# Performance work log

Hardware: AMD Instinct MI355X
Metric: run time of the kernel (lower is better)

Reference implementation:

```python
import jax, jax.numpy as jnp
import numpy as np

N = 100000          # nodes per type
D = 128             # embedding_dim
E_TREE = 100000     # intra-type tree edges
E_LINK = 1000000    # cross-type link edges
L = 2               # graph_num_layers
T = 4               # edge types: [dd, mm, dm, md]


def _sage(x_src, x_dst, ei, Wl, bl, Wr):
    """PyG SAGEConv(aggr='mean', normalize=False): lin_l(mean_j x_src_j) + lin_r(x_dst)."""
    n_dst = x_dst.shape[0]
    msg = x_src[ei[0]]                                                    # [E, D] gather
    ssum = jax.ops.segment_sum(msg, ei[1], num_segments=n_dst)            # [n_dst, D]
    cnt = jax.ops.segment_sum(jnp.ones((ei.shape[1],), x_src.dtype), ei[1], num_segments=n_dst)
    agg = ssum / jnp.maximum(cnt, 1.0)[:, None]                           # mean, safe for deg-0
    return agg @ Wl.T + bl + x_dst @ Wr.T


def _forward(x_d, x_m, e_dd, e_mm, e_dm, e_md, Wl, bl, Wr):
    num_layers = Wl.shape[0]
    for l in range(num_layers):
        # HeteroConv aggr='sum': sum conv outputs over edge types per dst node type
        nd = (_sage(x_d, x_d, e_dd, Wl[l, 0], bl[l, 0], Wr[l, 0])
              + _sage(x_m, x_d, e_md, Wl[l, 3], bl[l, 3], Wr[l, 3]))
        nm = (_sage(x_m, x_m, e_mm, Wl[l, 1], bl[l, 1], Wr[l, 1])
              + _sage(x_d, x_m, e_dm, Wl[l, 2], bl[l, 2], Wr[l, 2]))
        if l < num_layers - 1:
            nd, nm = jax.nn.relu(nd), jax.nn.relu(nm)
        x_d, x_m = nd, nm
    return jnp.stack([x_d, x_m])                                          # [2, N, D]


def setup_inputs() -> dict:
    key = jax.random.key(0)
    ks = jax.random.split(key, 9)
    scale = 1.0 / np.sqrt(D)
    return {
        "x_d": jax.random.normal(ks[0], (N, D), jnp.float32),
        "x_m": jax.random.normal(ks[1], (N, D), jnp.float32),
        "e_dd": jax.random.randint(ks[2], (2, E_TREE), 0, N, jnp.int64),
        "e_mm": jax.random.randint(ks[3], (2, E_TREE), 0, N, jnp.int64),
        "e_dm": jax.random.randint(ks[4], (2, E_LINK), 0, N, jnp.int64),
        "e_md": jax.random.randint(ks[5], (2, E_LINK), 0, N, jnp.int64),
        "Wl": jax.random.normal(ks[6], (L, T, D, D), jnp.float32) * scale,
        "bl": jax.random.normal(ks[7], (L, T, D), jnp.float32) * scale,
        "Wr": jax.random.normal(ks[8], (L, T, D, D), jnp.float32) * scale,
    }


def reference(x_d, x_m, e_dd, e_mm, e_dm, e_md, Wl, bl, Wr):
    return _forward(x_d, x_m, e_dd, e_mm, e_dm, e_md, Wl, bl, Wr)
```

## Files before the change

### kernel.cpp

```cpp
#include <hip/hip_runtime.h>

#define DD 128
#define KTOT 384
#define BM 64
#define BS_BITS 10
#define BS 1024
#define NBMAX 512
#define CHUNK 2048
#define CAP 12288

typedef __attribute__((ext_vector_type(8))) short short8;
typedef __attribute__((ext_vector_type(8))) unsigned short ushort8;
typedef __attribute__((ext_vector_type(4))) float floatx4;

__device__ __forceinline__ unsigned short f2b(float f) {
    union { float f; unsigned u; } v; v.f = f;
    return (unsigned short)((v.u + 0x7fffu + ((v.u >> 16) & 1u)) >> 16);
}
__device__ __forceinline__ float b2f(unsigned short u) {
    union { unsigned u; float f; } v; v.u = ((unsigned)u) << 16;
    return v.f;
}

__global__ __launch_bounds__(256) void detect_i32(const int* __restrict__ p, int nodd,
                                                  int* __restrict__ flag)
{
    int i = blockIdx.x * 256 + threadIdx.x;
    if (i < nodd && p[2 * i + 1] != 0) atomicOr(flag, 1);
}

__global__ __launch_bounds__(256) void cvt_bf16(const float* __restrict__ in,
                                                unsigned short* __restrict__ out, int n8)
{
    int i = blockIdx.x * 256 + threadIdx.x;
    if (i >= n8) return;
    float4 v0 = *(const float4*)(in + (size_t)i * 8);
    float4 v1 = *(const float4*)(in + (size_t)i * 8 + 4);
    ushort8 r;
    r[0]=f2b(v0.x); r[1]=f2b(v0.y); r[2]=f2b(v0.z); r[3]=f2b(v0.w);
    r[4]=f2b(v1.x); r[5]=f2b(v1.y); r[6]=f2b(v1.z); r[7]=f2b(v1.w);
    *(ushort8*)(out + (size_t)i * 8) = r;
}

__global__ __launch_bounds__(256) void build_wcomb(
    const float* __restrict__ Wl, const float* __restrict__ bl,
    const float* __restrict__ Wr, unsigned short* __restrict__ WTt, float* __restrict__ bc)
{
    int idx = blockIdx.x * 256 + threadIdx.x;
    if (idx < 2 * 2 * DD * KTOT) {
        int k  = idx % KTOT;
        int t1 = idx / KTOT;
        int i  = t1 & 127;
        int t2 = t1 >> 7;
        int dt = t2 & 1;
        int l  = t2 >> 1;
        int ta = dt ? 1 : 0;
        int tb = dt ? 2 : 3;
        float v;
        if (k < 128) {
            v = Wl[(((size_t)(l * 4 + ta) * 128 + i) << 7) + k];
        } else if (k < 256) {
            v = Wl[(((size_t)(l * 4 + tb) * 128 + i) << 7) + (k - 128)];
        } else {
            int kk = k - 256;
            v = Wr[(((size_t)(l * 4 + ta) * 128 + i) << 7) + kk]
              + Wr[(((size_t)(l * 4 + tb) * 128 + i) << 7) + kk];
        }
        int tidx = ((((i >> 4) * 12 + (k >> 5)) * 64) + (((k >> 3) & 3) * 16 + (i & 15))) * 8
                 + (k & 7);
        WTt[(size_t)t2 * (DD * KTOT) + tidx] = f2b(v);
    }
    if (idx < 512) {
        int i  = idx & 127;
        int t2 = idx >> 7;
        int dt = t2 & 1;
        int l  = t2 >> 1;
        int ta = dt ? 1 : 0;
        int tb = dt ? 2 : 3;
        bc[idx] = bl[(l * 4 + ta) * 128 + i] + bl[(l * 4 + tb) * 128 + i];
    }
}

__global__ __launch_bounds__(512) void bin_edges(
    const void* __restrict__ e0, const void* __restrict__ e1,
    const void* __restrict__ e2, const void* __restrict__ e3,
    int E0, int E1, int E2, int E3,
    const int* __restrict__ flag, int* __restrict__ bucket_fill,
    unsigned* __restrict__ stage,
    unsigned long long* __restrict__ ovf, int* __restrict__ ovf_cnt,
    int N, int nb)
{
    __shared__ unsigned sb_pack[CHUNK];
    __shared__ unsigned short sb_b[CHUNK];
    __shared__ int hist[NBMAX];
    __shared__ int offs[NBMAX];
    __shared__ int base[NBMAX];

    const int tid   = threadIdx.x;
    const int E_tot = E0 + E1 + E2 + E3;
    const int e_bas = blockIdx.x * CHUNK;
    const int e_end = min(e_bas + CHUNK, E_tot);
    const int cnt_e = e_end - e_bas;
    const int isI32 = *flag;

    for (int i = tid; i < nb; i += 512) hist[i] = 0;
    __syncthreads();

    unsigned my_pack[4];
    int my_b[4], my_r[4];
    #pragma unroll
    for (int u = 0; u < 4; ++u) {
        my_b[u] = -1;
        int e = e_bas + tid + u * 512;
        if (e < e_end) {
            const void* ep; int El, type, le = e;
            if (le < E0)              { ep = e0; El = E0; type = 0; }
            else if ((le -= E0) < E1) { ep = e1; El = E1; type = 1; }
            else if ((le -= E1) < E2) { ep = e2; El = E2; type = 2; }
            else                      { le -= E2; ep = e3; El = E3; type = 3; }
            int s, d;
            if (isI32) {
                s = ((const int*)ep)[le];
                d = ((const int*)ep)[(size_t)El + le];
            } else {
                s = (int)((const long long*)ep)[le];
                d = (int)((const long long*)ep)[(size_t)El + le];
            }
            int gnode = type * N + d;
            int b = gnode >> BS_BITS;
            my_b[u]    = b;
            my_pack[u] = ((unsigned)s << BS_BITS) | (unsigned)(gnode & (BS - 1));
            my_r[u]    = atomicAdd(&hist[b], 1);
        }
    }
    __syncthreads();

    offs[tid] = (tid < nb) ? hist[tid] : 0;
    __syncthreads();
    for (int d = 1; d < 512; d <<= 1) {
        int v = (tid >= d) ? offs[tid - d] : 0;
        __syncthreads();
        offs[tid] += v;
        __syncthreads();
    }
    if (tid < nb) {
        offs[tid] -= hist[tid];
        base[tid] = hist[tid] ? atomicAdd(&bucket_fill[tid], hist[tid]) : 0;
    }
    __syncthreads();

    #pragma unroll
    for (int u = 0; u < 4; ++u) {
        if (my_b[u] >= 0) {
            int pos = offs[my_b[u]] + my_r[u];
            sb_pack[pos] = my_pack[u];
            sb_b[pos]    = (unsigned short)my_b[u];
        }
    }
    __syncthreads();

    for (int pos = tid; pos < cnt_e; pos += 512) {
        int b = sb_b[pos];
        unsigned p = sb_pack[pos];
        int idx = base[b] + (pos - offs[b]);
        if (idx < CAP) {
            stage[(size_t)b * CAP + idx] = p;
        } else {
            int k = atomicAdd(ovf_cnt, 1);
            int gnode = (b << BS_BITS) | (int)(p & (BS - 1));
            ovf[k] = ((unsigned long long)(unsigned)gnode << 32) | (p >> BS_BITS);
        }
    }
}

__global__ __launch_bounds__(512) void scan_buckets(const int* __restrict__ fill, int nb,
                                                    int* __restrict__ base)
{
    __shared__ int s[512];
    const int tid = threadIdx.x;
    int v = (tid < nb) ? fill[tid] : 0;
    s[tid] = v;
    __syncthreads();
    for (int d = 1; d < 512; d <<= 1) {
        int u = (tid >= d) ? s[tid - d] : 0;
        __syncthreads();
        s[tid] += u;
        __syncthreads();
    }
    if (tid < nb) base[tid] = s[tid] - v;
}

__global__ __launch_bounds__(512) void fill_from_stage(
    const unsigned* __restrict__ stage, const int* __restrict__ bucket_fill,
    const int* __restrict__ bucket_base,
    const unsigned long long* __restrict__ ovf, const int* __restrict__ ovf_cnt,
    int* __restrict__ rp_all, float* __restrict__ inv_all, int* __restrict__ col, int n4)
{
    __shared__ int cl[BS];
    __shared__ int rl[BS];
    __shared__ int w[512];

    const int tid   = threadIdx.x;
    const int b     = blockIdx.x;
    const int node0 = b << BS_BITS;
    const int nn    = min(BS, n4 - node0);

    cl[tid] = 0; cl[tid + 512] = 0;
    __syncthreads();

    const int total  = bucket_fill[b];
    const int nstage = min(total, CAP);
    const unsigned* st = stage + (size_t)b * CAP;
    const int novf = *ovf_cnt;

    for (int j = tid; j < nstage; j += 512)
        atomicAdd(&cl[st[j] & (BS - 1)], 1);
    for (int k = tid; k < novf; k += 512) {
        int g = (int)(ovf[k] >> 32);
        if (g >= node0 && g < node0 + nn) atomicAdd(&cl[g - node0], 1);
    }
    __syncthreads();

    int a0 = cl[2 * tid], a1 = cl[2 * tid + 1];
    w[tid] = a0 + a1;
    __syncthreads();
    for (int d = 1; d < 512; d <<= 1) {
        int v = (tid >= d) ? w[tid - d] : 0;
        __syncthreads();
        w[tid] += v;
        __syncthreads();
    }
    int excl = w[tid] - a0 - a1;
    rl[2 * tid]     = excl;
    rl[2 * tid + 1] = excl + a0;
    __syncthreads();

    const int gbase = bucket_base[b];
    for (int i = tid; i < nn; i += 512) {
        rp_all[node0 + i] = gbase + rl[i];
        inv_all[node0 + i] = 1.0f / (float)max(cl[i], 1);
    }
    if (b == gridDim.x - 1 && tid == 0) rp_all[n4] = gbase + total;
    __syncthreads();

    for (int i = tid; i < BS; i += 512) cl[i] = gbase + rl[i];
    __syncthreads();

    for (int j = tid; j < nstage; j += 512) {
        unsigned p = st[j];
        int slot = atomicAdd(&cl[p & (BS - 1)], 1);
        col[slot] = (int)(p >> BS_BITS);
    }
    for (int k = tid; k < novf; k += 512) {
        unsigned long long p = ovf[k];
        int g = (int)(p >> 32);
        if (g >= node0 && g < node0 + nn) {
            int slot = atomicAdd(&cl[g - node0], 1);
            col[slot] = (int)(p & 0xffffffffu);
        }
    }
}

__global__ __launch_bounds__(256) void aggregate_all(
    const unsigned short* __restrict__ x, const int* __restrict__ rp,
    const float* __restrict__ inv, const int* __restrict__ col,
    unsigned short* __restrict__ At, int N)
{
    long long g = (long long)blockIdx.x * 256 + threadIdx.x;
    int node = (int)(g >> 4);
    int q    = (int)(g & 15);
    if (node >= 2 * N) return;

    const int isM  = node >= N;
    const int segA = node + (isM ? N : 0);
    const int segB = segA + N;
    const int selfbase  = isM ? N : 0;
    const int otherbase = N - selfbase;

    const int r16 = node >> 4;
    const int fr  = node & 15;
    unsigned short* tbase = At + ((size_t)r16 * 8 + (q >> 2)) * 512 + ((q & 3) * 16 + fr) * 8;

    const unsigned short* xs = x + (size_t)selfbase  * DD + q * 8;
    const unsigned short* xo = x + (size_t)otherbase * DD + q * 8;

    float accA[8], accB[8];
    #pragma unroll
    for (int t = 0; t < 8; ++t) { accA[t] = 0.f; accB[t] = 0.f; }

    int jA = rp[segA], eA = rp[segA + 1];
    int jB = rp[segB], eB = rp[segB + 1];

    while (jA + 4 <= eA && jB + 4 <= eB) {
        int a0 = col[jA], a1 = col[jA+1], a2 = col[jA+2], a3 = col[jA+3];
        int b0 = col[jB], b1 = col[jB+1], b2 = col[jB+2], b3 = col[jB+3];
        ushort8 va0 = *(const ushort8*)(xs + (size_t)a0 * DD);
        ushort8 va1 = *(const ushort8*)(xs + (size_t)a1 * DD);
        ushort8 va2 = *(const ushort8*)(xs + (size_t)a2 * DD);
        ushort8 va3 = *(const ushort8*)(xs + (size_t)a3 * DD);
        ushort8 vb0 = *(const ushort8*)(xo + (size_t)b0 * DD);
        ushort8 vb1 = *(const ushort8*)(xo + (size_t)b1 * DD);
        ushort8 vb2 = *(const ushort8*)(xo + (size_t)b2 * DD);
        ushort8 vb3 = *(const ushort8*)(xo + (size_t)b3 * DD);
        #pragma unroll
        for (int t = 0; t < 8; ++t) {
            accA[t] += (b2f(va0[t]) + b2f(va1[t])) + (b2f(va2[t]) + b2f(va3[t]));
            accB[t] += (b2f(vb0[t]) + b2f(vb1[t])) + (b2f(vb2[t]) + b2f(vb3[t]));
        }
        jA += 4; jB += 4;
    }
    while (jA + 4 <= eA) {
        int a0 = col[jA], a1 = col[jA+1], a2 = col[jA+2], a3 = col[jA+3];
        ushort8 va0 = *(const ushort8*)(xs + (size_t)a0 * DD);
        ushort8 va1 = *(const ushort8*)(xs + (size_t)a1 * DD);
        ushort8 va2 = *(const ushort8*)(xs + (size_t)a2 * DD);
        ushort8 va3 = *(const ushort8*)(xs + (size_t)a3 * DD);
        #pragma unroll
        for (int t = 0; t < 8; ++t)
            accA[t] += (b2f(va0[t]) + b2f(va1[t])) + (b2f(va2[t]) + b2f(va3[t]));
        jA += 4;
    }
    while (jB + 4 <= eB) {
        int b0 = col[jB], b1 = col[jB+1], b2 = col[jB+2], b3 = col[jB+3];
        ushort8 vb0 = *(const ushort8*)(xo + (size_t)b0 * DD);
        ushort8 vb1 = *(const ushort8*)(xo + (size_t)b1 * DD);
        ushort8 vb2 = *(const ushort8*)(xo + (size_t)b2 * DD);
        ushort8 vb3 = *(const ushort8*)(xo + (size_t)b3 * DD);
        #pragma unroll
        for (int t = 0; t < 8; ++t)
            accB[t] += (b2f(vb0[t]) + b2f(vb1[t])) + (b2f(vb2[t]) + b2f(vb3[t]));
        jB += 4;
    }
    for (; jA < eA; ++jA) {
        ushort8 v = *(const ushort8*)(xs + (size_t)col[jA] * DD);
        #pragma unroll
        for (int t = 0; t < 8; ++t) accA[t] += b2f(v[t]);
    }
    for (; jB < eB; ++jB) {
        ushort8 v = *(const ushort8*)(xo + (size_t)col[jB] * DD);
        #pragma unroll
        for (int t = 0; t < 8; ++t) accB[t] += b2f(v[t]);
    }

    float scA = inv[segA], scB = inv[segB];
    ushort8 rA, rB;
    #pragma unroll
    for (int t = 0; t < 8; ++t) { rA[t] = f2b(accA[t] * scA); rB[t] = f2b(accB[t] * scB); }
    *(ushort8*)(tbase)           = rA;
    *(ushort8*)(tbase + 4 * 512) = rB;
}

__global__ __launch_bounds__(256) void gemm_mfma(
    const unsigned short* __restrict__ At, const unsigned short* __restrict__ x,
    const unsigned short* __restrict__ WTt, const float* __restrict__ bc,
    void* __restrict__ outp, int relu, int write_f32, int N, int gd)
{
    const int tid = threadIdx.x;
    const int b   = blockIdx.x;
    const int isM = (b >= gd);
    const int row0   = isM ? N + (b - gd) * BM : b * BM;
    const int rowlim = isM ? 2 * N : N;
    const int tlim   = (rowlim >> 4) - 1;

    const unsigned short* WT   = WTt + (size_t)isM * DD * KTOT;
    const float*          bias = bc + isM * DD;

    const int wave = tid >> 6;
    const int lane = tid & 63;
    const int wr = (wave >> 1) * 32;
    const int wc = (wave & 1) * 64;
    const int fr  = lane & 15;
    const int fk8 = lane >> 4;

    int r16a = (row0 >> 4) + (wave >> 1) * 2;
    int r16b = r16a + 1;
    if (r16a > tlim) r16a = tlim;
    if (r16b > tlim) r16b = tlim;

    const unsigned short* Abase0 = At + (size_t)r16a * 8 * 512 + lane * 8;
    const unsigned short* Abase1 = At + (size_t)r16b * 8 * 512 + lane * 8;
    const unsigned short* Xbase0 = x + (size_t)(r16a * 16 + fr) * DD + fk8 * 8;
    const unsigned short* Xbase1 = x + (size_t)(r16b * 16 + fr) * DD + fk8 * 8;
    const unsigned short* Wbase  = WTt + (size_t)isM * DD * KTOT + (size_t)(wc >> 4) * 12 * 512 + lane * 8;

    floatx4 acc[2][4] = {};

    short8 a0c, a1c, a0n, a1n, bC[4], bN[4];
    a0c = *(const short8*)(Abase0);
    a1c = *(const short8*)(Abase1);
    #pragma unroll
    for (int c = 0; c < 4; ++c) bC[c] = *(const short8*)(Wbase + (size_t)c * 12 * 512);

    #pragma unroll
    for (int ks = 0; ks < 12; ++ks) {
        if (ks < 11) {
            int kn = ks + 1;
            if (kn < 8) {
                a0n = *(const short8*)(Abase0 + kn * 512);
                a1n = *(const short8*)(Abase1 + kn * 512);
            } else {
                a0n = *(const short8*)(Xbase0 + (kn - 8) * 32);
                a1n = *(const short8*)(Xbase1 + (kn - 8) * 32);
            }
            #pragma unroll
            for (int c = 0; c < 4; ++c) bN[c] = *(const short8*)(Wbase + (size_t)c * 12 * 512 + kn * 512);
        }
        #pragma unroll
        for (int c = 0; c < 4; ++c) {
            acc[0][c] = __builtin_amdgcn_mfma_f32_16x16x32_bf16(a0c, bC[c], acc[0][c], 0, 0, 0);
            acc[1][c] = __builtin_amdgcn_mfma_f32_16x16x32_bf16(a1c, bC[c], acc[1][c], 0, 0, 0);
        }
        a0c = a0n; a1c = a1n;
        #pragma unroll
        for (int c = 0; c < 4; ++c) bC[c] = bN[c];
    }

    float* outf = (float*)outp;
    unsigned short* outb = (unsigned short*)outp;
    const int rb = (lane >> 4) * 4;
    #pragma unroll
    for (int c = 0; c < 4; ++c) {
        int ocol = wc + c * 16 + fr;
        float bb = bias[ocol];
        #pragma unroll
        for (int m = 0; m < 2; ++m) {
            #pragma unroll
            for (int i = 0; i < 4; ++i) {
                int orow = row0 + wr + m * 16 + rb + i;
                if (orow >= rowlim) continue;
                float v = acc[m][c][i] + bb;
                if (relu) v = fmaxf(v, 0.f);
                if (write_f32) outf[(size_t)orow * DD + ocol] = v;
                else           outb[(size_t)orow * DD + ocol] = f2b(v);
            }
        }
    }
}

extern "C" void kernel_launch(void* const* d_in, const int* in_sizes, int n_in,
                              void* d_out, int out_size, void* d_ws, size_t ws_size,
                              hipStream_t stream)
{
    const float* x_d = (const float*)d_in[0];
    const float* x_m = (const float*)d_in[1];
    const float* Wl  = (const float*)d_in[6];
    const float* bl  = (const float*)d_in[7];
    const float* Wr  = (const float*)d_in[8];
    float* out = (float*)d_out;

    const int N    = in_sizes[0] / DD;
    const int E_dd = in_sizes[2] / 2;
    const int E_mm = in_sizes[3] / 2;
    const int E_dm = in_sizes[4] / 2;
    const int E_md = in_sizes[5] / 2;
    const int E_tot = E_dd + E_md + E_mm + E_dm;
    const int n4 = 4 * N;
    const int nb = (n4 + BS - 1) >> BS_BITS;
    const int M16 = (2 * N + 15) >> 4;

    char* ws = (char*)d_ws;
    size_t off = 0;
    auto alloc = [&](size_t bytes) {
        void* p = ws + off;
        off += (bytes + 255) & ~(size_t)255;
        return p;
    };
    unsigned short* xb    = (unsigned short*)alloc((size_t)2 * N * DD * 2);
    unsigned short* hb    = (unsigned short*)alloc((size_t)2 * N * DD * 2);
    unsigned short* At    = (unsigned short*)alloc((size_t)M16 * 8 * 512 * 2);
    float* inv_all = (float*)alloc((size_t)n4 * 4);
    int*   rp_all  = (int*)  alloc((size_t)(n4 + 1) * 4);
    int*   bucket_fill = (int*)alloc((size_t)NBMAX * 4);
    int*   bucket_base = (int*)alloc((size_t)NBMAX * 4);
    unsigned short* WTt = (unsigned short*)alloc((size_t)2 * 2 * DD * KTOT * 2);
    float* bc      = (float*)alloc((size_t)512 * 4);
    unsigned* stage = (unsigned*)alloc((size_t)nb * CAP * 4);
    int*   col     = (int*)alloc((size_t)E_tot * 4);
    unsigned long long* ovf = (unsigned long long*)alloc((size_t)(1 << 18) * 8);
    int*   ovf_cnt = (int*)alloc(256);
    int*   flag    = (int*)alloc(256);

    hipMemsetAsync(flag, 0, 256, stream);
    detect_i32<<<4, 256, 0, stream>>>((const int*)d_in[2], 1024, flag);

    const int n8 = N * DD / 8;
    cvt_bf16<<<(n8 + 255) / 256, 256, 0, stream>>>(x_d, xb, n8);
    cvt_bf16<<<(n8 + 255) / 256, 256, 0, stream>>>(x_m, xb + (size_t)N * DD, n8);

    hipMemsetAsync(bucket_fill, 0, (size_t)NBMAX * 4, stream);
    hipMemsetAsync(ovf_cnt, 0, 256, stream);
    const int nchunks = (E_tot + CHUNK - 1) / CHUNK;
    bin_edges<<<nchunks, 512, 0, stream>>>(
        d_in[2], d_in[5], d_in[3], d_in[4], E_dd, E_md, E_mm, E_dm,
        flag, bucket_fill, stage, ovf, ovf_cnt, N, nb);
    scan_buckets<<<1, 512, 0, stream>>>(bucket_fill, nb, bucket_base);
    fill_from_stage<<<nb, 512, 0, stream>>>(
        stage, bucket_fill, bucket_base, ovf, ovf_cnt, rp_all, inv_all, col, n4);

    build_wcomb<<<(2 * 2 * DD * KTOT + 255) / 256, 256, 0, stream>>>(Wl, bl, Wr, WTt, bc);

    const int agg_grid = (int)(((size_t)2 * N * 16 + 255) / 256);
    const int gd = (N + BM - 1) / BM;
    const int gemm_grid = 2 * gd;
    const unsigned short* xcur = xb;
    for (int l = 0; l < 2; ++l) {
        int relu = (l == 0);
        int wf32 = (l == 1);
        void* ob = (l == 1) ? (void*)out : (void*)hb;

        aggregate_all<<<agg_grid, 256, 0, stream>>>(xcur, rp_all, inv_all, col, At, N);
        gemm_mfma<<<gemm_grid, 256, 0, stream>>>(
            At, xcur, WTt + (size_t)l * 2 * DD * KTOT, bc + l * 2 * DD,
            ob, relu, wf32, N, gd);

        xcur = hb;
    }
}
```

Before: 428.8 us.

## Fuse neighbor aggregation into MFMA GEMM via shared-memory tile

Merges the separate aggregation and GEMM kernels into one kernel. Each block aggregates 16 destination nodes into an LDS tile and then runs the bf16 MFMA GEMM directly from it. This removes the global round trip of the aggregated At buffer and one launch per layer. In exchange, each block now does only 16 rows, so every block reloads the full weight matrix, the GEMM loses its prefetch pipelining, and the grid is much larger.

```diff
diff --git a/kernel.cpp b/kernel.cpp
--- a/kernel.cpp
+++ b/kernel.cpp
@@ -2,12 +2,12 @@
 
 #define DD 128
 #define KTOT 384
-#define BM 64
 #define BS_BITS 10
 #define BS 1024
 #define NBMAX 512
 #define CHUNK 2048
 #define CAP 12288
+#define LROW 264
 
 typedef __attribute__((ext_vector_type(8))) short short8;
 typedef __attribute__((ext_vector_type(8))) unsigned short ushort8;
@@ -261,178 +261,141 @@
     }
 }
 
-__global__ __launch_bounds__(256) void aggregate_all(
+__global__ __launch_bounds__(256) void gemm_agg_fused(
     const unsigned short* __restrict__ x, const int* __restrict__ rp,
     const float* __restrict__ inv, const int* __restrict__ col,
-    unsigned short* __restrict__ At, int N)
-{
-    long long g = (long long)blockIdx.x * 256 + threadIdx.x;
-    int node = (int)(g >> 4);
-    int q    = (int)(g & 15);
-    if (node >= 2 * N) return;
-
-    const int isM  = node >= N;
-    const int segA = node + (isM ? N : 0);
-    const int segB = segA + N;
-    const int selfbase  = isM ? N : 0;
-    const int otherbase = N - selfbase;
-
-    const int r16 = node >> 4;
-    const int fr  = node & 15;
-    unsigned short* tbase = At + ((size_t)r16 * 8 + (q >> 2)) * 512 + ((q & 3) * 16 + fr) * 8;
-
-    const unsigned short* xs = x + (size_t)selfbase  * DD + q * 8;
-    const unsigned short* xo = x + (size_t)otherbase * DD + q * 8;
-
-    float accA[8], accB[8];
-    #pragma unroll
-    for (int t = 0; t < 8; ++t) { accA[t] = 0.f; accB[t] = 0.f; }
-
-    int jA = rp[segA], eA = rp[segA + 1];
-    int jB = rp[segB], eB = rp[segB + 1];
-
-    while (jA + 4 <= eA && jB + 4 <= eB) {
-        int a0 = col[jA], a1 = col[jA+1], a2 = col[jA+2], a3 = col[jA+3];
-        int b0 = col[jB], b1 = col[jB+1], b2 = col[jB+2], b3 = col[jB+3];
-        ushort8 va0 = *(const ushort8*)(xs + (size_t)a0 * DD);
-        ushort8 va1 = *(const ushort8*)(xs + (size_t)a1 * DD);
-        ushort8 va2 = *(const ushort8*)(xs + (size_t)a2 * DD);
-        ushort8 va3 = *(const ushort8*)(xs + (size_t)a3 * DD);
-        ushort8 vb0 = *(const ushort8*)(xo + (size_t)b0 * DD);
-        ushort8 vb1 = *(const ushort8*)(xo + (size_t)b1 * DD);
-        ushort8 vb2 = *(const ushort8*)(xo + (size_t)b2 * DD);
-        ushort8 vb3 = *(const ushort8*)(xo + (size_t)b3 * DD);
-        #pragma unroll
-        for (int t = 0; t < 8; ++t) {
-            accA[t] += (b2f(va0[t]) + b2f(va1[t])) + (b2f(va2[t]) + b2f(va3[t]));
-            accB[t] += (b2f(vb0[t]) + b2f(vb1[t])) + (b2f(vb2[t]) + b2f(vb3[t]));
-        }
-        jA += 4; jB += 4;
-    }
-    while (jA + 4 <= eA) {
-        int a0 = col[jA], a1 = col[jA+1], a2 = col[jA+2], a3 = col[jA+3];
-        ushort8 va0 = *(const ushort8*)(xs + (size_t)a0 * DD);
-        ushort8 va1 = *(const ushort8*)(xs + (size_t)a1 * DD);
-        ushort8 va2 = *(const ushort8*)(xs + (size_t)a2 * DD);
-        ushort8 va3 = *(const ushort8*)(xs + (size_t)a3 * DD);
-        #pragma unroll
-        for (int t = 0; t < 8; ++t)
-            accA[t] += (b2f(va0[t]) + b2f(va1[t])) + (b2f(va2[t]) + b2f(va3[t]));
-        jA += 4;
-    }
-    while (jB + 4 <= eB) {
-        int b0 = col[jB], b1 = col[jB+1], b2 = col[jB+2], b3 = col[jB+3];
-        ushort8 vb0 = *(const ushort8*)(xo + (size_t)b0 * DD);
-        ushort8 vb1 = *(const ushort8*)(xo + (size_t)b1 * DD);
-        ushort8 vb2 = *(const ushort8*)(xo + (size_t)b2 * DD);
-        ushort8 vb3 = *(const ushort8*)(xo + (size_t)b3 * DD);
-        #pragma unroll
-        for (int t = 0; t < 8; ++t)
-            accB[t] += (b2f(vb0[t]) + b2f(vb1[t])) + (b2f(vb2[t]) + b2f(vb3[t]));
-        jB += 4;
-    }
-    for (; jA < eA; ++jA) {
-        ushort8 v = *(const ushort8*)(xs + (size_t)col[jA] * DD);
-        #pragma unroll
-        for (int t = 0; t < 8; ++t) accA[t] += b2f(v[t]);
-    }
-    for (; jB < eB; ++jB) {
-        ushort8 v = *(const ushort8*)(xo + (size_t)col[jB] * DD);
-        #pragma unroll
-        for (int t = 0; t < 8; ++t) accB[t] += b2f(v[t]);
-    }
-
-    float scA = inv[segA], scB = inv[segB];
-    ushort8 rA, rB;
-    #pragma unroll
-    for (int t = 0; t < 8; ++t) { rA[t] = f2b(accA[t] * scA); rB[t] = f2b(accB[t] * scB); }
-    *(ushort8*)(tbase)           = rA;
-    *(ushort8*)(tbase + 4 * 512) = rB;
-}
-
-__global__ __launch_bounds__(256) void gemm_mfma(
-    const unsigned short* __restrict__ At, const unsigned short* __restrict__ x,
-    const unsigned short* __restrict__ WTt, const float* __restrict__ bc,
-    void* __restrict__ outp, int relu, int write_f32, int N, int gd)
-{
+    const unsigned short* __restrict__ WTt, const float* __restrict__ bcb,
+    void* __restrict__ outp, int relu, int write_f32, int N, int gd16)
+{
+    __shared__ unsigned short As[16 * LROW];
     const int tid = threadIdx.x;
     const int b   = blockIdx.x;
-    const int isM = (b >= gd);
-    const int row0   = isM ? N + (b - gd) * BM : b * BM;
+    const int isM = (b >= gd16) ? 1 : 0;
+    const int base = isM ? N + (b - gd16) * 16 : b * 16;
     const int rowlim = isM ? 2 * N : N;
-    const int tlim   = (rowlim >> 4) - 1;
 
     const unsigned short* WT   = WTt + (size_t)isM * DD * KTOT;
-    const float*          bias = bc + isM * DD;
+    const float*          bias = bcb + isM * DD;
+
+    {
+        const int nl = tid >> 4;
+        const int q  = tid & 15;
+        int node = base + nl;
+        if (node > rowlim - 1) node = rowlim - 1;
+        const int segA = node + (isM ? N : 0);
+        const int segB = segA + N;
+        const int selfbase  = isM ? N : 0;
+        const int otherbase = N - selfbase;
+        const unsigned short* xs = x + (size_t)selfbase  * DD + q * 8;
+        const unsigned short* xo = x + (size_t)otherbase * DD + q * 8;
+
+        float accA[8], accB[8];
+        #pragma unroll
+        for (int t = 0; t < 8; ++t) { accA[t] = 0.f; accB[t] = 0.f; }
+
+        int jA = rp[segA], eA = rp[segA + 1];
+        int jB = rp[segB], eB = rp[segB + 1];
+
+        while (jA + 4 <= eA && jB + 4 <= eB) {
+            int a0 = col[jA], a1 = col[jA+1], a2 = col[jA+2], a3 = col[jA+3];
+            int b0 = col[jB], b1 = col[jB+1], b2 = col[jB+2], b3 = col[jB+3];
+            ushort8 va0 = *(const ushort8*)(xs + (size_t)a0 * DD);
+            ushort8 va1 = *(const ushort8*)(xs + (size_t)a1 * DD);
+            ushort8 va2 = *(const ushort8*)(xs + (size_t)a2 * DD);
+            ushort8 va3 = *(const ushort8*)(xs + (size_t)a3 * DD);
+            ushort8 vb0 = *(const ushort8*)(xo + (size_t)b0 * DD);
+            ushort8 vb1 = *(const ushort8*)(xo + (size_t)b1 * DD);
+            ushort8 vb2 = *(const ushort8*)(xo + (size_t)b2 * DD);
+            ushort8 vb3 = *(const ushort8*)(xo + (size_t)b3 * DD);
+            #pragma unroll
+            for (int t = 0; t < 8; ++t) {
+                accA[t] += (b2f(va0[t]) + b2f(va1[t])) + (b2f(va2[t]) + b2f(va3[t]));
+                accB[t] += (b2f(vb0[t]) + b2f(vb1[t])) + (b2f(vb2[t]) + b2f(vb3[t]));
+            }
+            jA += 4; jB += 4;
+        }
+        while (jA + 4 <= eA) {
+            int a0 = col[jA], a1 = col[jA+1], a2 = col[jA+2], a3 = col[jA+3];
+            ushort8 va0 = *(const ushort8*)(xs + (size_t)a0 * DD);
+            ushort8 va1 = *(const ushort8*)(xs + (size_t)a1 * DD);
+            ushort8 va2 = *(const ushort8*)(xs + (size_t)a2 * DD);
+            ushort8 va3 = *(const ushort8*)(xs + (size_t)a3 * DD);
+            #pragma unroll
+            for (int t = 0; t < 8; ++t)
+                accA[t] += (b2f(va0[t]) + b2f(va1[t])) + (b2f(va2[t]) + b2f(va3[t]));
+            jA += 4;
+        }
+        while (jB + 4 <= eB) {
+            int b0 = col[jB], b1 = col[jB+1], b2 = col[jB+2], b3 = col[jB+3];
+            ushort8 vb0 = *(const ushort8*)(xo + (size_t)b0 * DD);
+            ushort8 vb1 = *(const ushort8*)(xo + (size_t)b1 * DD);
+            ushort8 vb2 = *(const ushort8*)(xo + (size_t)b2 * DD);
+            ushort8 vb3 = *(const ushort8*)(xo + (size_t)b3 * DD);
+            #pragma unroll
+            for (int t = 0; t < 8; ++t)
+                accB[t] += (b2f(vb0[t]) + b2f(vb1[t])) + (b2f(vb2[t]) + b2f(vb3[t]));
+            jB += 4;
+        }
+        for (; jA < eA; ++jA) {
+            ushort8 v = *(const ushort8*)(xs + (size_t)col[jA] * DD);
+            #pragma unroll
+            for (int t = 0; t < 8; ++t) accA[t] += b2f(v[t]);
+        }
+        for (; jB < eB; ++jB) {
+            ushort8 v = *(const ushort8*)(xo + (size_t)col[jB] * DD);
+            #pragma unroll
+            for (int t = 0; t < 8; ++t) accB[t] += b2f(v[t]);
+        }
+
+        float scA = inv[segA], scB = inv[segB];
+        ushort8 rA, rB;
+        #pragma unroll
+        for (int t = 0; t < 8; ++t) { rA[t] = f2b(accA[t] * scA); rB[t] = f2b(accB[t] * scB); }
+        *(ushort8*)(&As[nl * LROW + q * 8])        = rA;
+        *(ushort8*)(&As[nl * LROW + (16 + q) * 8]) = rB;
+    }
+    __syncthreads();
 
     const int wave = tid >> 6;
     const int lane = tid & 63;
-    const int wr = (wave >> 1) * 32;
-    const int wc = (wave & 1) * 64;
     const int fr  = lane & 15;
     const int fk8 = lane >> 4;
-
-    int r16a = (row0 >> 4) + (wave >> 1) * 2;
-    int r16b = r16a + 1;
-    if (r16a > tlim) r16a = tlim;
-    if (r16b > tlim) r16b = tlim;
-
-    const unsigned short* Abase0 = At + (size_t)r16a * 8 * 512 + lane * 8;
-    const unsigned short* Abase1 = At + (size_t)r16b * 8 * 512 + lane * 8;
-    const unsigned short* Xbase0 = x + (size_t)(r16a * 16 + fr) * DD + fk8 * 8;
-    const unsigned short* Xbase1 = x + (size_t)(r16b * 16 + fr) * DD + fk8 * 8;
-    const unsigned short* Wbase  = WTt + (size_t)isM * DD * KTOT + (size_t)(wc >> 4) * 12 * 512 + lane * 8;
-
-    floatx4 acc[2][4] = {};
-
-    short8 a0c, a1c, a0n, a1n, bC[4], bN[4];
-    a0c = *(const short8*)(Abase0);
-    a1c = *(const short8*)(Abase1);
+    const int wc  = wave * 32;
+
+    int xrow = base + fr;
+    if (xrow > rowlim - 1) xrow = rowlim - 1;
+    const unsigned short* Xb  = x + (size_t)xrow * DD + fk8 * 8;
+    const unsigned short* Wb0 = WT + (size_t)((wc >> 4) + 0) * 12 * 512 + lane * 8;
+    const unsigned short* Wb1 = WT + (size_t)((wc >> 4) + 1) * 12 * 512 + lane * 8;
+
+    floatx4 acc0 = {}, acc1 = {};
     #pragma unroll
-    for (int c = 0; c < 4; ++c) bC[c] = *(const short8*)(Wbase + (size_t)c * 12 * 512);
-
-    #pragma unroll
-    for (int ks = 0; ks < 12; ++ks) {
-        if (ks < 11) {
-            int kn = ks + 1;
-            if (kn < 8) {
-                a0n = *(const short8*)(Abase0 + kn * 512);
-                a1n = *(const short8*)(Abase1 + kn * 512);
-            } else {
-                a0n = *(const short8*)(Xbase0 + (kn - 8) * 32);
-                a1n = *(const short8*)(Xbase1 + (kn - 8) * 32);
-            }
-            #pragma unroll
-            for (int c = 0; c < 4; ++c) bN[c] = *(const short8*)(Wbase + (size_t)c * 12 * 512 + kn * 512);
-        }
-        #pragma unroll
-        for (int c = 0; c < 4; ++c) {
-            acc[0][c] = __builtin_amdgcn_mfma_f32_16x16x32_bf16(a0c, bC[c], acc[0][c], 0, 0, 0);
-            acc[1][c] = __builtin_amdgcn_mfma_f32_16x16x32_bf16(a1c, bC[c], acc[1][c], 0, 0, 0);
-        }
-        a0c = a0n; a1c = a1n;
-        #pragma unroll
-        for (int c = 0; c < 4; ++c) bC[c] = bN[c];
+    for (int k32 = 0; k32 < 12; ++k32) {
+        short8 a;
+        if (k32 < 8) a = *(const short8*)(&As[fr * LROW + (k32 * 4 + fk8) * 8]);
+        else         a = *(const short8*)(Xb + (k32 - 8) * 32);
+        short8 b0 = *(const short8*)(Wb0 + k32 * 512);
+        short8 b1 = *(const short8*)(Wb1 + k32 * 512);
+        acc0 = __builtin_amdgcn_mfma_f32_16x16x32_bf16(a, b0, acc0, 0, 0, 0);
+        acc1 = __builtin_amdgcn_mfma_f32_16x16x32_bf16(a, b1, acc1, 0, 0, 0);
     }
 
     float* outf = (float*)outp;
     unsigned short* outb = (unsigned short*)outp;
-    const int rb = (lane >> 4) * 4;
+    const int rb = fk8 * 4;
     #pragma unroll
-    for (int c = 0; c < 4; ++c) {
+    for (int c = 0; c < 2; ++c) {
+        const floatx4& ac = c ? acc1 : acc0;
         int ocol = wc + c * 16 + fr;
         float bb = bias[ocol];
         #pragma unroll
-        for (int m = 0; m < 2; ++m) {
-            #pragma unroll
-            for (int i = 0; i < 4; ++i) {
-                int orow = row0 + wr + m * 16 + rb + i;
-                if (orow >= rowlim) continue;
-                float v = acc[m][c][i] + bb;
-                if (relu) v = fmaxf(v, 0.f);
-                if (write_f32) outf[(size_t)orow * DD + ocol] = v;
-                else           outb[(size_t)orow * DD + ocol] = f2b(v);
-            }
+        for (int i = 0; i < 4; ++i) {
+            int orow = base + rb + i;
+            if (orow >= rowlim) continue;
+            float v = ac[i] + bb;
+            if (relu) v = fmaxf(v, 0.f);
+            if (write_f32) outf[(size_t)orow * DD + ocol] = v;
+            else           outb[(size_t)orow * DD + ocol] = f2b(v);
         }
     }
 }
@@ -456,7 +419,6 @@
     const int E_tot = E_dd + E_md + E_mm + E_dm;
     const int n4 = 4 * N;
     const int nb = (n4 + BS - 1) >> BS_BITS;
-    const int M16 = (2 * N + 15) >> 4;
 
     char* ws = (char*)d_ws;
     size_t off = 0;
@@ -467,7 +429,6 @@
     };
     unsigned short* xb    = (unsigned short*)alloc((size_t)2 * N * DD * 2);
     unsigned short* hb    = (unsigned short*)alloc((size_t)2 * N * DD * 2);
-    unsigned short* At    = (unsigned short*)alloc((size_t)M16 * 8 * 512 * 2);
     float* inv_all = (float*)alloc((size_t)n4 * 4);
     int*   rp_all  = (int*)  alloc((size_t)(n4 + 1) * 4);
     int*   bucket_fill = (int*)alloc((size_t)NBMAX * 4);
@@ -499,19 +460,18 @@
 
     build_wcomb<<<(2 * 2 * DD * KTOT + 255) / 256, 256, 0, stream>>>(Wl, bl, Wr, WTt, bc);
 
-    const int agg_grid = (int)(((size_t)2 * N * 16 + 255) / 256);
-    const int gd = (N + BM - 1) / BM;
-    const int gemm_grid = 2 * gd;
+    const int gd16 = (N + 15) / 16;
+    const int fused_grid = 2 * gd16;
     const unsigned short* xcur = xb;
     for (int l = 0; l < 2; ++l) {
         int relu = (l == 0);
         int wf32 = (l == 1);
         void* ob = (l == 1) ? (void*)out : (void*)hb;
 
-        aggregate_all<<<agg_grid, 256, 0, stream>>>(xcur, rp_all, inv_all, col, At, N);
-        gemm_mfma<<<gemm_grid, 256, 0, stream>>>(
-            At, xcur, WTt + (size_t)l * 2 * DD * KTOT, bc + l * 2 * DD,
-            ob, relu, wf32, N, gd);
+        gemm_agg_fused<<<fused_grid, 256, 0, stream>>>(
+            xcur, rp_all, inv_all, col,
+            WTt + (size_t)l * 2 * DD * KTOT, bc + l * 2 * DD,
+            ob, relu, wf32, N, gd16);
 
         xcur = hb;
     }
```

New measurement: 434.1 us. About the same (+1.2%).
